# Performance work log

Hardware: AMD Instinct MI355X
Metric: run time of the kernel (lower is better)

The kernel has to match this reference:

```python
import jax, jax.numpy as jnp
import numpy as np

O, G, GS = 8192, 64, 128   # out_features, n_groups, group_size
I = G * GS                 # in_features = 8192
RANK = 128                 # svd_rank
RESULT_SHAPE = (O, I)


def setup_inputs() -> dict:
    key = jax.random.key(0)
    k1, k2, k3, k4, k5 = jax.random.split(key, 5)
    weight = jax.random.randint(k1, (O, G, GS), 0, 256, dtype=jnp.int32)
    # realistic small per-group scales and zero points
    scale = jax.random.uniform(k2, (O, G, 1), dtype=jnp.float32) * 0.01 + 1e-4
    zero_point = jax.random.normal(k3, (O, G, 1), dtype=jnp.float32) * 0.05
    svd_up = jax.random.normal(k4, (O, RANK), dtype=jnp.float32) * 0.02
    svd_down = jax.random.normal(k5, (RANK, I), dtype=jnp.float32) * 0.02
    return {
        "weight": weight,
        "scale": scale,
        "zero_point": zero_point,
        "svd_up": svd_up,
        "svd_down": svd_down,
    }


def reference(weight, scale, zero_point, svd_up, svd_down):
    # addcmul: zero_point + weight * scale  (broadcast over group dim)
    result = zero_point + weight.astype(scale.dtype) * scale      # [O, G, GS]
    result = result.reshape(RESULT_SHAPE)                          # [O, I]
    # low-rank SVD correction: result += svd_up @ svd_down (addmm_)
    result = result + jnp.matmul(svd_up, svd_down)                 # [O, I]
    return result.astype(jnp.float32)                              # final dtype cast
```

## Files before the change

kernel.cpp:

```cpp
#include <hip/hip_runtime.h>
#include <hip/hip_bf16.h>

#define O_DIM 8192
#define I_DIM 8192
#define G_DIM 64
#define RANK  128

typedef __bf16 bf16x8 __attribute__((ext_vector_type(8)));
typedef __bf16 bf16x4 __attribute__((ext_vector_type(4)));
typedef float  f32x4  __attribute__((ext_vector_type(4)));

__global__ void k_convert_up(const float* __restrict__ up, __bf16* __restrict__ A_bf) {
    size_t t = (size_t)blockIdx.x * blockDim.x + threadIdx.x;
    const float4* in4 = (const float4*)up;
    float4 v = in4[t];
    bf16x4 o = { (__bf16)v.x, (__bf16)v.y, (__bf16)v.z, (__bf16)v.w };
    *(bf16x4*)(A_bf + 4 * t) = o;
}

__global__ void k_transpose_down(const float* __restrict__ down, __bf16* __restrict__ Bt) {
    __shared__ __bf16 tile[64][132];
    int tid = threadIdx.x;
    int ib  = blockIdx.x * 64;
    int il  = tid & 63;
    int k4  = tid >> 6;
    for (int kk = 0; kk < 32; ++kk) {
        int k = kk * 4 + k4;
        tile[il][k] = (__bf16)down[(size_t)k * I_DIM + ib + il];
    }
    __syncthreads();
    uint2* dst = (uint2*)(Bt + (size_t)ib * RANK);
    #pragma unroll
    for (int jj = 0; jj < 8; ++jj) {
        int f   = (jj * 256 + tid) * 4;
        int i_l = f >> 7;
        int k_l = f & 127;
        dst[jj * 256 + tid] = *(const uint2*)&tile[i_l][k_l];
    }
}

__global__ __launch_bounds__(256)
void k_main(const int* __restrict__ weight, const float* __restrict__ scale,
            const float* __restrict__ zp, const __bf16* __restrict__ A_bf,
            const __bf16* __restrict__ Bt_bf, float* __restrict__ out) {
    __shared__ float s_lds[128];
    __shared__ float z_lds[128];
    int tid = threadIdx.x;
    int g       = blockIdx.x;
    int rowbase = blockIdx.y * 128;
    int colbase = g * 128;

    if (tid < 128) s_lds[tid]       = scale[(size_t)(rowbase + tid) * G_DIM + g];
    else           z_lds[tid - 128] = zp[(size_t)(rowbase + tid - 128) * G_DIM + g];
    __syncthreads();

    int w    = tid >> 6;
    int lane = tid & 63;
    int l15  = lane & 15;
    int quad = lane >> 4;
    int wrow = (w >> 1) * 64;
    int wcol = (w & 1) * 64;

    const __bf16* Ap = A_bf  + (size_t)(rowbase + wrow + l15) * RANK + quad * 8;
    const __bf16* Bp = Bt_bf + (size_t)(colbase + wcol + l15) * RANK + quad * 8;

    f32x4 acc[4][4];
    #pragma unroll
    for (int rb = 0; rb < 4; ++rb)
        #pragma unroll
        for (int cb = 0; cb < 4; ++cb)
            acc[rb][cb] = (f32x4){0.f, 0.f, 0.f, 0.f};

    #pragma unroll
    for (int kc = 0; kc < 4; ++kc) {
        bf16x8 af[4], bfr[4];
        #pragma unroll
        for (int rb = 0; rb < 4; ++rb)
            af[rb] = *(const bf16x8*)(Ap + rb * 16 * RANK + kc * 32);
        #pragma unroll
        for (int cb = 0; cb < 4; ++cb)
            bfr[cb] = *(const bf16x8*)(Bp + cb * 16 * RANK + kc * 32);
        #pragma unroll
        for (int rb = 0; rb < 4; ++rb)
            #pragma unroll
            for (int cb = 0; cb < 4; ++cb)
                acc[rb][cb] = __builtin_amdgcn_mfma_f32_16x16x32_bf16(
                    af[rb], bfr[cb], acc[rb][cb], 0, 0, 0);
    }

    int orow0 = wrow + quad * 4;
    size_t base = (size_t)(rowbase + orow0) * I_DIM + colbase + wcol + l15;
    #pragma unroll
    for (int rb = 0; rb < 4; ++rb) {
        int wv[16];
        #pragma unroll
        for (int r = 0; r < 4; ++r)
            #pragma unroll
            for (int cb = 0; cb < 4; ++cb)
                wv[r * 4 + cb] = weight[base + (size_t)(rb * 16 + r) * I_DIM + cb * 16];
        #pragma unroll
        for (int r = 0; r < 4; ++r) {
            int ol  = orow0 + rb * 16 + r;
            float s = s_lds[ol];
            float z = z_lds[ol];
            #pragma unroll
            for (int cb = 0; cb < 4; ++cb) {
                float v = fmaf((float)wv[r * 4 + cb], s, z) + acc[rb][cb][r];
                out[base + (size_t)(rb * 16 + r) * I_DIM + cb * 16] = v;
            }
        }
    }
}

extern "C" void kernel_launch(void* const* d_in, const int* in_sizes, int n_in,
                              void* d_out, int out_size, void* d_ws, size_t ws_size,
                              hipStream_t stream) {
    const int*   weight = (const int*)d_in[0];
    const float* scale  = (const float*)d_in[1];
    const float* zp     = (const float*)d_in[2];
    const float* up     = (const float*)d_in[3];
    const float* down   = (const float*)d_in[4];
    float* out = (float*)d_out;

    __bf16* A_bf  = (__bf16*)d_ws;
    __bf16* Bt_bf = A_bf + (size_t)O_DIM * RANK;

    k_convert_up<<<1024, 256, 0, stream>>>(up, A_bf);
    k_transpose_down<<<128, 256, 0, stream>>>(down, Bt_bf);

    dim3 grid(64, 64);
    k_main<<<grid, 256, 0, stream>>>(weight, scale, zp, A_bf, Bt_bf, out);
}
```

Measured before the change: 494.9 us.

## Prefetch weight tile into LDS asynchronously during MFMA, load scales into registers

Each block now issues async global_load_lds copies of its full 128x128 int32 weight tile into shared memory before running the low-rank MFMA. The weight fetch therefore overlaps with the matmul instead of being issued afterwards as scattered per-lane loads. Scale and zero-point values go straight into registers, and launch bounds request 2 blocks per CU. The 64KB LDS per block limits occupancy, and the LDS reads in the epilogue may hit bank conflicts.

```diff
diff --git a/kernel.cpp b/kernel.cpp
--- a/kernel.cpp
+++ b/kernel.cpp
@@ -39,27 +39,45 @@
     }
 }
 
-__global__ __launch_bounds__(256)
+__global__ __launch_bounds__(256, 2)
 void k_main(const int* __restrict__ weight, const float* __restrict__ scale,
             const float* __restrict__ zp, const __bf16* __restrict__ A_bf,
             const __bf16* __restrict__ Bt_bf, float* __restrict__ out) {
-    __shared__ float s_lds[128];
-    __shared__ float z_lds[128];
+    __shared__ int w_lds[128 * 128];
     int tid = threadIdx.x;
     int g       = blockIdx.x;
     int rowbase = blockIdx.y * 128;
     int colbase = g * 128;
 
-    if (tid < 128) s_lds[tid]       = scale[(size_t)(rowbase + tid) * G_DIM + g];
-    else           z_lds[tid - 128] = zp[(size_t)(rowbase + tid - 128) * G_DIM + g];
-    __syncthreads();
-
     int w    = tid >> 6;
     int lane = tid & 63;
+
+    {
+        const int* gsrc = weight + (size_t)(rowbase + (lane >> 5)) * I_DIM
+                        + colbase + ((lane & 31) * 4);
+        #pragma unroll
+        for (int jj = 0; jj < 16; ++jj) {
+            int j = w * 16 + jj;
+            __builtin_amdgcn_global_load_lds(
+                (const __attribute__((address_space(1))) void*)(gsrc + (size_t)(2 * j) * I_DIM),
+                (__attribute__((address_space(3))) void*)(&w_lds[j * 256]),
+                16, 0, 0);
+        }
+    }
+
     int l15  = lane & 15;
     int quad = lane >> 4;
     int wrow = (w >> 1) * 64;
     int wcol = (w & 1) * 64;
+    int orow0 = wrow + quad * 4;
+
+    float sv[16], zv[16];
+    #pragma unroll
+    for (int i = 0; i < 16; ++i) {
+        int row = rowbase + orow0 + (i >> 2) * 16 + (i & 3);
+        sv[i] = scale[(size_t)row * G_DIM + g];
+        zv[i] = zp[(size_t)row * G_DIM + g];
+    }
 
     const __bf16* Ap = A_bf  + (size_t)(rowbase + wrow + l15) * RANK + quad * 8;
     const __bf16* Bp = Bt_bf + (size_t)(colbase + wcol + l15) * RANK + quad * 8;
@@ -88,24 +106,20 @@
                     af[rb], bfr[cb], acc[rb][cb], 0, 0, 0);
     }
 
-    int orow0 = wrow + quad * 4;
+    __syncthreads();
+
+    int    widx = orow0 * 128 + wcol + l15;
     size_t base = (size_t)(rowbase + orow0) * I_DIM + colbase + wcol + l15;
     #pragma unroll
     for (int rb = 0; rb < 4; ++rb) {
-        int wv[16];
-        #pragma unroll
-        for (int r = 0; r < 4; ++r)
-            #pragma unroll
-            for (int cb = 0; cb < 4; ++cb)
-                wv[r * 4 + cb] = weight[base + (size_t)(rb * 16 + r) * I_DIM + cb * 16];
         #pragma unroll
         for (int r = 0; r < 4; ++r) {
-            int ol  = orow0 + rb * 16 + r;
-            float s = s_lds[ol];
-            float z = z_lds[ol];
+            float s = sv[rb * 4 + r];
+            float z = zv[rb * 4 + r];
             #pragma unroll
             for (int cb = 0; cb < 4; ++cb) {
-                float v = fmaf((float)wv[r * 4 + cb], s, z) + acc[rb][cb][r];
+                float v = fmaf((float)w_lds[widx + (rb * 16 + r) * 128 + cb * 16], s, z)
+                        + acc[rb][cb][r];
                 out[base + (size_t)(rb * 16 + r) * I_DIM + cb * 16] = v;
             }
         }
```

Result: faster. 479.8 us (-3.0%).

## Swap MFMA operands for row-major vector IO and prefetch weights before GEMM

Applied to the files above, without the earlier changes.

Swaps the A/B operands of the MFMA so each lane holds four consecutive output columns of one row. Weight loads and output stores then become 16-byte vectors instead of scalar strided accesses. Scale and zero-point are now read per lane straight from global memory, removing the LDS staging and the barrier. All weight loads are issued before the MFMA loop so their latency overlaps compute, and launch bounds request two blocks per CU, which adds register pressure from the 64 prefetched weight registers.

```diff
diff --git a/kernel.cpp b/kernel.cpp
--- a/kernel.cpp
+++ b/kernel.cpp
@@ -9,6 +9,7 @@
 typedef __bf16 bf16x8 __attribute__((ext_vector_type(8)));
 typedef __bf16 bf16x4 __attribute__((ext_vector_type(4)));
 typedef float  f32x4  __attribute__((ext_vector_type(4)));
+typedef int    i32x4  __attribute__((ext_vector_type(4)));
 
 __global__ void k_convert_up(const float* __restrict__ up, __bf16* __restrict__ A_bf) {
     size_t t = (size_t)blockIdx.x * blockDim.x + threadIdx.x;
@@ -39,20 +40,14 @@
     }
 }
 
-__global__ __launch_bounds__(256)
+__global__ __launch_bounds__(256, 2)
 void k_main(const int* __restrict__ weight, const float* __restrict__ scale,
             const float* __restrict__ zp, const __bf16* __restrict__ A_bf,
             const __bf16* __restrict__ Bt_bf, float* __restrict__ out) {
-    __shared__ float s_lds[128];
-    __shared__ float z_lds[128];
     int tid = threadIdx.x;
     int g       = blockIdx.x;
     int rowbase = blockIdx.y * 128;
     int colbase = g * 128;
-
-    if (tid < 128) s_lds[tid]       = scale[(size_t)(rowbase + tid) * G_DIM + g];
-    else           z_lds[tid - 128] = zp[(size_t)(rowbase + tid - 128) * G_DIM + g];
-    __syncthreads();
 
     int w    = tid >> 6;
     int lane = tid & 63;
@@ -64,6 +59,35 @@
     const __bf16* Ap = A_bf  + (size_t)(rowbase + wrow + l15) * RANK + quad * 8;
     const __bf16* Bp = Bt_bf + (size_t)(colbase + wcol + l15) * RANK + quad * 8;
 
+    bf16x8 af[2][4], bfr[2][4];
+    #pragma unroll
+    for (int j = 0; j < 2; ++j)
+        #pragma unroll
+        for (int rb = 0; rb < 4; ++rb) {
+            af[j][rb]  = *(const bf16x8*)(Ap + rb * 16 * RANK + j * 32);
+            bfr[j][rb] = *(const bf16x8*)(Bp + rb * 16 * RANK + j * 32);
+        }
+    __builtin_amdgcn_sched_barrier(0);
+
+    float sv[4], zv[4];
+    #pragma unroll
+    for (int rb = 0; rb < 4; ++rb) {
+        int row = rowbase + wrow + rb * 16 + l15;
+        sv[rb] = scale[(size_t)row * G_DIM + g];
+        zv[rb] = zp[(size_t)row * G_DIM + g];
+    }
+    __builtin_amdgcn_sched_barrier(0);
+
+    i32x4 wt[4][4];
+    const int* Wp = weight + (size_t)(rowbase + wrow + l15) * I_DIM
+                  + colbase + wcol + quad * 4;
+    #pragma unroll
+    for (int rb = 0; rb < 4; ++rb)
+        #pragma unroll
+        for (int cb = 0; cb < 4; ++cb)
+            wt[rb][cb] = *(const i32x4*)(Wp + (size_t)(rb * 16) * I_DIM + cb * 16);
+    __builtin_amdgcn_sched_barrier(0);
+
     f32x4 acc[4][4];
     #pragma unroll
     for (int rb = 0; rb < 4; ++rb)
@@ -72,42 +96,46 @@
             acc[rb][cb] = (f32x4){0.f, 0.f, 0.f, 0.f};
 
     #pragma unroll
-    for (int kc = 0; kc < 4; ++kc) {
-        bf16x8 af[4], bfr[4];
-        #pragma unroll
-        for (int rb = 0; rb < 4; ++rb)
-            af[rb] = *(const bf16x8*)(Ap + rb * 16 * RANK + kc * 32);
-        #pragma unroll
-        for (int cb = 0; cb < 4; ++cb)
-            bfr[cb] = *(const bf16x8*)(Bp + cb * 16 * RANK + kc * 32);
+    for (int j = 0; j < 2; ++j)
         #pragma unroll
         for (int rb = 0; rb < 4; ++rb)
             #pragma unroll
             for (int cb = 0; cb < 4; ++cb)
                 acc[rb][cb] = __builtin_amdgcn_mfma_f32_16x16x32_bf16(
-                    af[rb], bfr[cb], acc[rb][cb], 0, 0, 0);
-    }
+                    bfr[j][cb], af[j][rb], acc[rb][cb], 0, 0, 0);
+    __builtin_amdgcn_sched_barrier(0);
 
-    int orow0 = wrow + quad * 4;
-    size_t base = (size_t)(rowbase + orow0) * I_DIM + colbase + wcol + l15;
+    #pragma unroll
+    for (int j = 0; j < 2; ++j)
+        #pragma unroll
+        for (int rb = 0; rb < 4; ++rb) {
+            af[j][rb]  = *(const bf16x8*)(Ap + rb * 16 * RANK + (2 + j) * 32);
+            bfr[j][rb] = *(const bf16x8*)(Bp + rb * 16 * RANK + (2 + j) * 32);
+        }
+    __builtin_amdgcn_sched_barrier(0);
+
+    #pragma unroll
+    for (int j = 0; j < 2; ++j)
+        #pragma unroll
+        for (int rb = 0; rb < 4; ++rb)
+            #pragma unroll
+            for (int cb = 0; cb < 4; ++cb)
+                acc[rb][cb] = __builtin_amdgcn_mfma_f32_16x16x32_bf16(
+                    bfr[j][cb], af[j][rb], acc[rb][cb], 0, 0, 0);
+    __builtin_amdgcn_sched_barrier(0);
+
+    size_t obase = (size_t)(rowbase + wrow + l15) * I_DIM + colbase + wcol + quad * 4;
     #pragma unroll
     for (int rb = 0; rb < 4; ++rb) {
-        int wv[16];
+        float s = sv[rb];
+        float z = zv[rb];
         #pragma unroll
-        for (int r = 0; r < 4; ++r)
+        for (int cb = 0; cb < 4; ++cb) {
+            f32x4 v;
             #pragma unroll
-            for (int cb = 0; cb < 4; ++cb)
-                wv[r * 4 + cb] = weight[base + (size_t)(rb * 16 + r) * I_DIM + cb * 16];
-        #pragma unroll
-        for (int r = 0; r < 4; ++r) {
-            int ol  = orow0 + rb * 16 + r;
-            float s = s_lds[ol];
-            float z = z_lds[ol];
-            #pragma unroll
-            for (int cb = 0; cb < 4; ++cb) {
-                float v = fmaf((float)wv[r * 4 + cb], s, z) + acc[rb][cb][r];
-                out[base + (size_t)(rb * 16 + r) * I_DIM + cb * 16] = v;
-            }
+            for (int e = 0; e < 4; ++e)
+                v[e] = fmaf((float)wt[rb][cb][e], s, z) + acc[rb][cb][e];
+            *(f32x4*)(out + obase + (size_t)(rb * 16) * I_DIM + cb * 16) = v;
         }
     }
 }
```

Result: faster. 482.8 us (-2.4%).
